# Optimization experiments

Hardware: AMD Instinct MI355X
Metric: run time of the kernel (lower is better)

The kernel has to match this reference:

```python
import jax, jax.numpy as jnp
import numpy as np

ALPHA = 0.2          # LeakyReLU negative slope
NEG_INF = -9e15      # mask value used by the original module
B, L, D, F_IN, F_OUT = 16, 256, 128, 64, 64


def setup_inputs() -> dict:
    key = jax.random.key(0)
    k1, k2, k3, k4 = jax.random.split(key, 4)
    h = jax.random.normal(k1, (B, L, D, F_IN), dtype=jnp.float32)
    adj = jax.random.randint(k2, (B, L, D, D), 0, 2, dtype=jnp.int32)
    # xavier_uniform(gain=1.414) bounds
    bW = 1.414 * np.sqrt(6.0 / (F_IN + F_OUT))
    W = jax.random.uniform(k3, (F_IN, F_OUT), dtype=jnp.float32, minval=-bW, maxval=bW)
    ba = 1.414 * np.sqrt(6.0 / (2 * F_OUT + 1))
    a = jax.random.uniform(k4, (2 * F_OUT, 1), dtype=jnp.float32, minval=-ba, maxval=ba)
    return {"h": h, "adj": adj, "W": W, "a": a}


def reference(h, adj, W, a):
    # h: [B,L,D,F_in], adj: [B,L,D,D]
    Wh = jnp.einsum('bldf,fo->bldo', h, W)              # [B,L,D,F_out]
    a1 = a[:F_OUT, 0]                                    # dots the "source" node i
    a2 = a[F_OUT:, 0]                                    # dots the "target" node j
    e_i = Wh @ a1                                        # [B,L,D]
    e_j = Wh @ a2                                        # [B,L,D]
    e = e_i[..., :, None] + e_j[..., None, :]            # [B,L,D,D] pairwise scores
    e = jnp.where(e > 0, e, ALPHA * e)                   # LeakyReLU
    att = jnp.where(adj > 0, e, NEG_INF)
    att = jax.nn.softmax(att, axis=-1)                   # dropout=eval mode (no-op)
    h_prime = jnp.einsum('bldk,blko->bldo', att, Wh)     # [B,L,D,F_out]
    return h_prime
```

## Files before the change

### kernel.cpp

```cpp
#include <hip/hip_runtime.h>

constexpr int D_   = 128;
constexpr int FIN  = 64;
constexpr int FOUT = 64;
constexpr float ALPHA = 0.2f;

typedef _Float16 f16x8 __attribute__((ext_vector_type(8)));
typedef float    f32x4 __attribute__((ext_vector_type(4)));

__global__ __launch_bounds__(256, 4) void gat_kernel(
    const float* __restrict__ hg, const int* __restrict__ adjg,
    const float* __restrict__ Wg, const float* __restrict__ ag,
    float* __restrict__ outg)
{
    __shared__ __align__(16) unsigned short sX[128 * 64];
    __shared__ float sEi[D_];
    __shared__ __align__(16) float sEj[D_];
    __shared__ float sL[D_];
    __shared__ float sMxW[4];

    const int tid  = threadIdx.x;
    const int lane = tid & 63;
    const int w    = tid >> 6;
    const int g    = lane >> 4;
    const int m16  = lane & 15;
    const int row0 = w * 32 + m16;

    const long bl = blockIdx.x;
    const float* hp   = hg   + bl * (long)(D_ * FIN);
    const int*   adjp = adjg + bl * (long)(D_ * D_);
    float*       outp = outg + bl * (long)(D_ * FOUT);

    char* xb = (char*)sX;

    f16x8 ha[2][2];
    #pragma unroll
    for (int mt = 0; mt < 2; ++mt)
        #pragma unroll
        for (int kt = 0; kt < 2; ++kt) {
            const float* hb = hp + (w * 32 + mt * 16 + m16) * 64 + kt * 32 + g * 8;
            float4 v0 = *(const float4*)hb;
            float4 v1 = *(const float4*)(hb + 4);
            ha[mt][kt][0] = (_Float16)v0.x; ha[mt][kt][1] = (_Float16)v0.y;
            ha[mt][kt][2] = (_Float16)v0.z; ha[mt][kt][3] = (_Float16)v0.w;
            ha[mt][kt][4] = (_Float16)v1.x; ha[mt][kt][5] = (_Float16)v1.y;
            ha[mt][kt][6] = (_Float16)v1.z; ha[mt][kt][7] = (_Float16)v1.w;
        }
    int4 areg[4];
    {
        const int* a0 = adjp + row0 * D_ + g * 8;
        areg[0] = *(const int4*)(a0);
        areg[1] = *(const int4*)(a0 + 4);
        areg[2] = *(const int4*)(a0 + 16 * D_);
        areg[3] = *(const int4*)(a0 + 16 * D_ + 4);
    }
    {
        const int f0 = (tid & 15) * 4;
        const int o0 = (tid >> 4) * 4;
        float4 r0 = *(const float4*)&Wg[(f0 + 0) * 64 + o0];
        float4 r1 = *(const float4*)&Wg[(f0 + 1) * 64 + o0];
        float4 r2 = *(const float4*)&Wg[(f0 + 2) * 64 + o0];
        float4 r3 = *(const float4*)&Wg[(f0 + 3) * 64 + o0];
        float col[4][4] = {{r0.x, r1.x, r2.x, r3.x}, {r0.y, r1.y, r2.y, r3.y},
                           {r0.z, r1.z, r2.z, r3.z}, {r0.w, r1.w, r2.w, r3.w}};
        #pragma unroll
        for (int c = 0; c < 4; ++c) {
            int o = o0 + c;
            union { _Float16 h[4]; uint2 u; } cv;
            cv.h[0] = (_Float16)col[c][0]; cv.h[1] = (_Float16)col[c][1];
            cv.h[2] = (_Float16)col[c][2]; cv.h[3] = (_Float16)col[c][3];
            int off = (o * 128 + f0 * 2) ^ ((o & 7) << 4);
            *(uint2*)(xb + off) = cv.u;
        }
    }
    __syncthreads();

    f16x8 wf[2][4];
    #pragma unroll
    for (int kt = 0; kt < 2; ++kt)
        #pragma unroll
        for (int nt = 0; nt < 4; ++nt) {
            int o = nt * 16 + m16;
            wf[kt][nt] = *(const f16x8*)(xb + ((o * 128 + kt * 64 + g * 16) ^ ((o & 7) << 4)));
        }

    f32x4 acc[2][4];
    #pragma unroll
    for (int mt = 0; mt < 2; ++mt)
        #pragma unroll
        for (int nt = 0; nt < 4; ++nt) acc[mt][nt] = (f32x4){0.f, 0.f, 0.f, 0.f};

    #pragma unroll
    for (int kt = 0; kt < 2; ++kt)
        #pragma unroll
        for (int mt = 0; mt < 2; ++mt)
            #pragma unroll
            for (int nt = 0; nt < 4; ++nt)
                acc[mt][nt] = __builtin_amdgcn_mfma_f32_16x16x32_f16(ha[mt][kt], wf[kt][nt], acc[mt][nt], 0, 0, 0);
    __syncthreads();

    {
        float a1v[4], a2v[4];
        #pragma unroll
        for (int nt = 0; nt < 4; ++nt) {
            a1v[nt] = ag[nt * 16 + m16];
            a2v[nt] = ag[FOUT + nt * 16 + m16];
        }
        float wmax = -3.0e38f;
        #pragma unroll
        for (int mt = 0; mt < 2; ++mt) {
            #pragma unroll
            for (int r = 0; r < 4; ++r) {
                float ei = 0.f, ej = 0.f;
                #pragma unroll
                for (int nt = 0; nt < 4; ++nt) {
                    float v = acc[mt][nt][r];
                    ei += v * a1v[nt];
                    ej += v * a2v[nt];
                }
                #pragma unroll
                for (int s = 1; s < 16; s <<= 1) {
                    ei += __shfl_xor(ei, s);
                    ej += __shfl_xor(ej, s);
                }
                int row = w * 32 + mt * 16 + g * 4 + r;
                if (m16 == 0) { sEi[row] = ei; sEj[row] = ej; }
                wmax = fmaxf(wmax, ej);
            }
        }
        wmax = fmaxf(wmax, __shfl_xor(wmax, 16));
        wmax = fmaxf(wmax, __shfl_xor(wmax, 32));
        if (lane == 0) sMxW[w] = wmax;

        #pragma unroll
        for (int mt = 0; mt < 2; ++mt) {
            int j0r = w * 32 + mt * 16 + g * 4;
            #pragma unroll
            for (int nt = 0; nt < 4; ++nt) {
                int o = nt * 16 + m16;
                union { _Float16 h[4]; uint2 u; } cv;
                cv.h[0] = (_Float16)acc[mt][nt][0];
                cv.h[1] = (_Float16)acc[mt][nt][1];
                cv.h[2] = (_Float16)acc[mt][nt][2];
                cv.h[3] = (_Float16)acc[mt][nt][3];
                int off = (o * 256 + j0r * 2) ^ ((o & 7) << 4);
                *(uint2*)(xb + off) = cv.u;
            }
        }
    }
    __syncthreads();

    #pragma unroll
    for (int mt = 0; mt < 2; ++mt)
        #pragma unroll
        for (int nt = 0; nt < 4; ++nt) acc[mt][nt] = (f32x4){0.f, 0.f, 0.f, 0.f};

    const float ei0 = sEi[row0];
    const float ei1 = sEi[row0 + 16];
    const float mxj = fmaxf(fmaxf(sMxW[0], sMxW[1]), fmaxf(sMxW[2], sMxW[3]));
    float t0 = ei0 + mxj, t1 = ei1 + mxj;
    const float mi0 = t0 > 0.f ? t0 : ALPHA * t0;
    const float mi1 = t1 > 0.f ? t1 : ALPHA * t1;
    float lp0 = 0.f, lp1 = 0.f;

    const int* aprow0 = adjp + row0 * D_ + g * 8;
    const int* aprow1 = aprow0 + 16 * D_;

    #pragma unroll
    for (int jt = 0; jt < 4; ++jt) {
        const int j0 = jt * 32;
        float4 ejA = *(const float4*)&sEj[j0 + g * 8];
        float4 ejB = *(const float4*)&sEj[j0 + g * 8 + 4];
        float ejv[8] = {ejA.x, ejA.y, ejA.z, ejA.w, ejB.x, ejB.y, ejB.z, ejB.w};
        int aa0[8] = {areg[0].x, areg[0].y, areg[0].z, areg[0].w,
                      areg[1].x, areg[1].y, areg[1].z, areg[1].w};
        int aa1[8] = {areg[2].x, areg[2].y, areg[2].z, areg[2].w,
                      areg[3].x, areg[3].y, areg[3].z, areg[3].w};
        f16x8 pa0, pa1;
        #pragma unroll
        for (int q = 0; q < 8; ++q) {
            float e0 = ei0 + ejv[q];
            e0 = e0 > 0.f ? e0 : ALPHA * e0;
            float p0 = (aa0[q] > 0) ? __expf(e0 - mi0) : 0.f;
            lp0 += p0;
            pa0[q] = (_Float16)p0;
            float e1 = ei1 + ejv[q];
            e1 = e1 > 0.f ? e1 : ALPHA * e1;
            float p1 = (aa1[q] > 0) ? __expf(e1 - mi1) : 0.f;
            lp1 += p1;
            pa1[q] = (_Float16)p1;
        }
        if (jt < 3) {
            const int* n0 = aprow0 + (jt + 1) * 32;
            const int* n1 = aprow1 + (jt + 1) * 32;
            areg[0] = *(const int4*)(n0);
            areg[1] = *(const int4*)(n0 + 4);
            areg[2] = *(const int4*)(n1);
            areg[3] = *(const int4*)(n1 + 4);
        }
        f16x8 wb[4];
        #pragma unroll
        for (int nt = 0; nt < 4; ++nt) {
            int o = nt * 16 + m16;
            wb[nt] = *(const f16x8*)(xb + ((o * 256 + j0 * 2 + g * 16) ^ ((o & 7) << 4)));
        }
        #pragma unroll
        for (int nt = 0; nt < 4; ++nt) {
            acc[0][nt] = __builtin_amdgcn_mfma_f32_16x16x32_f16(pa0, wb[nt], acc[0][nt], 0, 0, 0);
            acc[1][nt] = __builtin_amdgcn_mfma_f32_16x16x32_f16(pa1, wb[nt], acc[1][nt], 0, 0, 0);
        }
    }

    lp0 += __shfl_xor(lp0, 16); lp0 += __shfl_xor(lp0, 32);
    lp1 += __shfl_xor(lp1, 16); lp1 += __shfl_xor(lp1, 32);
    if (g == 0) {
        sL[row0]      = lp0;
        sL[row0 + 16] = lp1;
    }

    #pragma unroll
    for (int mtx = 0; mtx < 2; ++mtx) {
        #pragma unroll
        for (int r = 0; r < 4; ++r) {
            int row = w * 32 + mtx * 16 + g * 4 + r;
            float inv = 1.0f / sL[row];
            #pragma unroll
            for (int nt = 0; nt < 4; ++nt)
                outp[row * 64 + nt * 16 + m16] = acc[mtx][nt][r] * inv;
        }
    }
}

extern "C" void kernel_launch(void* const* d_in, const int* in_sizes, int n_in,
                              void* d_out, int out_size, void* d_ws, size_t ws_size,
                              hipStream_t stream) {
    const float* h   = (const float*)d_in[0];
    const int*   adj = (const int*)d_in[1];
    const float* W   = (const float*)d_in[2];
    const float* a   = (const float*)d_in[3];
    float*       out = (float*)d_out;
    gat_kernel<<<dim3(16 * 256), dim3(256), 0, stream>>>(h, adj, W, a, out);
}
```

Measured before the change: 473.9 us.

## Precompute adjacency bitmask in a separate pass and consume bits in attention kernel

Adds a pre-pass kernel that packs the int32 adjacency matrix into 32-bit masks per thread slot, stored in the workspace. The main kernel then loads two mask words instead of streaming int4 adjacency rows during the softmax loop, and hoists the W loads earlier. The full adjacency is still read once by the pre-pass, so this adds a kernel launch and extra mask write/read traffic in exchange for a lighter main loop.

```diff
diff --git a/kernel.cpp b/kernel.cpp
--- a/kernel.cpp
+++ b/kernel.cpp
@@ -8,10 +8,34 @@
 typedef _Float16 f16x8 __attribute__((ext_vector_type(8)));
 typedef float    f32x4 __attribute__((ext_vector_type(4)));
 
+__global__ __launch_bounds__(256) void adj_mask_kernel(
+    const int* __restrict__ adj, unsigned* __restrict__ M)
+{
+    const int i   = blockIdx.x * 256 + threadIdx.x;
+    const int bl  = i >> 9;
+    const int idx = i & 511;
+    const int g   = idx >> 7;
+    const int row = idx & 127;
+    const int* p  = adj + (long)bl * (D_ * D_) + row * D_ + g * 8;
+    unsigned m = 0u;
+    #pragma unroll
+    for (int jt = 0; jt < 4; ++jt) {
+        int4 a = *(const int4*)(p + jt * 32);
+        int4 b = *(const int4*)(p + jt * 32 + 4);
+        const int base = jt * 8;
+        m |= ((unsigned)(a.x > 0) << (base + 0)) | ((unsigned)(a.y > 0) << (base + 1))
+           | ((unsigned)(a.z > 0) << (base + 2)) | ((unsigned)(a.w > 0) << (base + 3))
+           | ((unsigned)(b.x > 0) << (base + 4)) | ((unsigned)(b.y > 0) << (base + 5))
+           | ((unsigned)(b.z > 0) << (base + 6)) | ((unsigned)(b.w > 0) << (base + 7));
+    }
+    M[i] = m;
+}
+
+template<bool USE_MASK>
 __global__ __launch_bounds__(256, 4) void gat_kernel(
     const float* __restrict__ hg, const int* __restrict__ adjg,
     const float* __restrict__ Wg, const float* __restrict__ ag,
-    float* __restrict__ outg)
+    const unsigned* __restrict__ Mg, float* __restrict__ outg)
 {
     __shared__ __align__(16) unsigned short sX[128 * 64];
     __shared__ float sEi[D_];
@@ -32,6 +56,27 @@
     float*       outp = outg + bl * (long)(D_ * FOUT);
 
     char* xb = (char*)sX;
+
+    unsigned mask0 = 0u, mask1 = 0u;
+    int4 areg[4];
+    if constexpr (USE_MASK) {
+        const unsigned* mp = Mg + bl * 512 + g * 128;
+        mask0 = mp[row0];
+        mask1 = mp[row0 + 16];
+    } else {
+        const int* a0 = adjp + row0 * D_ + g * 8;
+        areg[0] = *(const int4*)(a0);
+        areg[1] = *(const int4*)(a0 + 4);
+        areg[2] = *(const int4*)(a0 + 16 * D_);
+        areg[3] = *(const int4*)(a0 + 16 * D_ + 4);
+    }
+
+    const int f0 = (tid & 15) * 4;
+    const int o0 = (tid >> 4) * 4;
+    float4 wr0 = *(const float4*)&Wg[(f0 + 0) * 64 + o0];
+    float4 wr1 = *(const float4*)&Wg[(f0 + 1) * 64 + o0];
+    float4 wr2 = *(const float4*)&Wg[(f0 + 2) * 64 + o0];
+    float4 wr3 = *(const float4*)&Wg[(f0 + 3) * 64 + o0];
 
     f16x8 ha[2][2];
     #pragma unroll
@@ -46,23 +91,10 @@
             ha[mt][kt][4] = (_Float16)v1.x; ha[mt][kt][5] = (_Float16)v1.y;
             ha[mt][kt][6] = (_Float16)v1.z; ha[mt][kt][7] = (_Float16)v1.w;
         }
-    int4 areg[4];
+
     {
-        const int* a0 = adjp + row0 * D_ + g * 8;
-        areg[0] = *(const int4*)(a0);
-        areg[1] = *(const int4*)(a0 + 4);
-        areg[2] = *(const int4*)(a0 + 16 * D_);
-        areg[3] = *(const int4*)(a0 + 16 * D_ + 4);
-    }
-    {
-        const int f0 = (tid & 15) * 4;
-        const int o0 = (tid >> 4) * 4;
-        float4 r0 = *(const float4*)&Wg[(f0 + 0) * 64 + o0];
-        float4 r1 = *(const float4*)&Wg[(f0 + 1) * 64 + o0];
-        float4 r2 = *(const float4*)&Wg[(f0 + 2) * 64 + o0];
-        float4 r3 = *(const float4*)&Wg[(f0 + 3) * 64 + o0];
-        float col[4][4] = {{r0.x, r1.x, r2.x, r3.x}, {r0.y, r1.y, r2.y, r3.y},
-                           {r0.z, r1.z, r2.z, r3.z}, {r0.w, r1.w, r2.w, r3.w}};
+        float col[4][4] = {{wr0.x, wr1.x, wr2.x, wr3.x}, {wr0.y, wr1.y, wr2.y, wr3.y},
+                           {wr0.z, wr1.z, wr2.z, wr3.z}, {wr0.w, wr1.w, wr2.w, wr3.w}};
         #pragma unroll
         for (int c = 0; c < 4; ++c) {
             int o = o0 + c;
@@ -172,31 +204,44 @@
         float4 ejA = *(const float4*)&sEj[j0 + g * 8];
         float4 ejB = *(const float4*)&sEj[j0 + g * 8 + 4];
         float ejv[8] = {ejA.x, ejA.y, ejA.z, ejA.w, ejB.x, ejB.y, ejB.z, ejB.w};
-        int aa0[8] = {areg[0].x, areg[0].y, areg[0].z, areg[0].w,
-                      areg[1].x, areg[1].y, areg[1].z, areg[1].w};
-        int aa1[8] = {areg[2].x, areg[2].y, areg[2].z, areg[2].w,
-                      areg[3].x, areg[3].y, areg[3].z, areg[3].w};
+        bool b0[8], b1[8];
+        if constexpr (USE_MASK) {
+            #pragma unroll
+            for (int q = 0; q < 8; ++q) {
+                b0[q] = (mask0 >> (jt * 8 + q)) & 1u;
+                b1[q] = (mask1 >> (jt * 8 + q)) & 1u;
+            }
+        } else {
+            int aa0[8] = {areg[0].x, areg[0].y, areg[0].z, areg[0].w,
+                          areg[1].x, areg[1].y, areg[1].z, areg[1].w};
+            int aa1[8] = {areg[2].x, areg[2].y, areg[2].z, areg[2].w,
+                          areg[3].x, areg[3].y, areg[3].z, areg[3].w};
+            #pragma unroll
+            for (int q = 0; q < 8; ++q) { b0[q] = aa0[q] > 0; b1[q] = aa1[q] > 0; }
+        }
         f16x8 pa0, pa1;
         #pragma unroll
         for (int q = 0; q < 8; ++q) {
             float e0 = ei0 + ejv[q];
             e0 = e0 > 0.f ? e0 : ALPHA * e0;
-            float p0 = (aa0[q] > 0) ? __expf(e0 - mi0) : 0.f;
+            float p0 = b0[q] ? __expf(e0 - mi0) : 0.f;
             lp0 += p0;
             pa0[q] = (_Float16)p0;
             float e1 = ei1 + ejv[q];
             e1 = e1 > 0.f ? e1 : ALPHA * e1;
-            float p1 = (aa1[q] > 0) ? __expf(e1 - mi1) : 0.f;
+            float p1 = b1[q] ? __expf(e1 - mi1) : 0.f;
             lp1 += p1;
             pa1[q] = (_Float16)p1;
         }
-        if (jt < 3) {
-            const int* n0 = aprow0 + (jt + 1) * 32;
-            const int* n1 = aprow1 + (jt + 1) * 32;
-            areg[0] = *(const int4*)(n0);
-            areg[1] = *(const int4*)(n0 + 4);
-            areg[2] = *(const int4*)(n1);
-            areg[3] = *(const int4*)(n1 + 4);
+        if constexpr (!USE_MASK) {
+            if (jt < 3) {
+                const int* n0 = aprow0 + (jt + 1) * 32;
+                const int* n1 = aprow1 + (jt + 1) * 32;
+                areg[0] = *(const int4*)(n0);
+                areg[1] = *(const int4*)(n0 + 4);
+                areg[2] = *(const int4*)(n1);
+                areg[3] = *(const int4*)(n1 + 4);
+            }
         }
         f16x8 wb[4];
         #pragma unroll
@@ -239,5 +284,13 @@
     const float* W   = (const float*)d_in[2];
     const float* a   = (const float*)d_in[3];
     float*       out = (float*)d_out;
-    gat_kernel<<<dim3(16 * 256), dim3(256), 0, stream>>>(h, adj, W, a, out);
+    const size_t mask_bytes = (size_t)(16 * 256) * 512 * sizeof(unsigned);
+    const bool use_mask = (d_ws != nullptr) && (ws_size >= mask_bytes);
+    if (use_mask) {
+        unsigned* M = (unsigned*)d_ws;
+        adj_mask_kernel<<<dim3(16 * 256 * 512 / 256), dim3(256), 0, stream>>>(adj, M);
+        gat_kernel<true><<<dim3(16 * 256), dim3(256), 0, stream>>>(h, adj, W, a, M, out);
+    } else {
+        gat_kernel<false><<<dim3(16 * 256), dim3(256), 0, stream>>>(h, adj, W, a, nullptr, out);
+    }
 }
```

Measured after the change: 486.3 us. +2.6%, slower.
